# Performance work log

Measured on AMD Instinct MI355X. Metric: run time of the kernel, lower is better.

Reference implementation:

```python
import jax, jax.numpy as jnp
import numpy as np

N_NODES = 100000
N_EDGES = 1_600_000
D = 64


def setup_inputs() -> dict:
    key = jax.random.key(0)
    ks = jax.random.split(key, 10)
    features = jax.random.normal(ks[0], (N_NODES, D), dtype=jnp.float32)
    src = jax.random.randint(ks[1], (N_EDGES,), 0, N_NODES, dtype=jnp.int64)
    dst = jax.random.randint(ks[2], (N_EDGES,), 0, N_NODES, dtype=jnp.int64)
    s = 1.0 / np.sqrt(D)
    W0 = jax.random.uniform(ks[3], (D, D), jnp.float32, -s, s)
    b0 = jnp.zeros((D,), jnp.float32)
    W1 = jax.random.uniform(ks[4], (D, D), jnp.float32, -s, s)
    b1 = jnp.zeros((D,), jnp.float32)
    W2 = jax.random.uniform(ks[5], (D, D), jnp.float32, -s, s)
    b2 = jnp.zeros((D,), jnp.float32)
    return {"features": features, "src": src, "dst": dst,
            "W0": W0, "b0": b0, "W1": W1, "b1": b1, "W2": W2, "b2": b2}


def _graph_conv_left(h, src, dst, deg_inv, W, b, act):
    # norm='left': scale source features by 1/out_degree, then copy-sum aggregate
    h = h * deg_inv[:, None]          # [N, d]
    msgs = h[src]                     # [E, d] gather
    agg = jax.ops.segment_sum(msgs, dst, num_segments=N_NODES)  # [N, d]
    out = agg @ W + b
    return act(out) if act is not None else out


def reference(features, src, dst, W0, b0, W1, b1, W2, b2):
    # out-degree with clamp(min=1), as in DGL GraphConv
    deg = jax.ops.segment_sum(jnp.ones((N_EDGES,), jnp.float32), src,
                              num_segments=N_NODES)
    deg_inv = 1.0 / jnp.maximum(deg, 1.0)
    h = _graph_conv_left(features, src, dst, deg_inv, W0, b0, jax.nn.relu)
    h = _graph_conv_left(h, src, dst, deg_inv, W1, b1, jax.nn.relu)
    h = _graph_conv_left(h, src, dst, deg_inv, W2, b2, None)
    mN = jnp.mean(h, axis=0, keepdims=True)  # readout_nodes op='mean', single graph -> [1, d]
    return (h, mN)
```

## Files before the change

### kernel.cpp

```cpp
#include <hip/hip_runtime.h>
#include <hip/hip_fp16.h>

#define D 64
#define NBUK 391
#define NBIN (2 * NBUK)
#define CHUNK 8192
#define PBSTRIDE 256

__global__ __launch_bounds__(256) void phase1_kernel(const int* __restrict__ src,
                                                     const int* __restrict__ dst,
                                                     int* __restrict__ per_block, int E) {
    __shared__ int h[NBIN];
    int tid = (int)threadIdx.x;
    for (int j = tid; j < NBIN; j += 256) h[j] = 0;
    __syncthreads();
    int base = blockIdx.x * CHUNK;
    int cnt = min(CHUNK, E - base);
    for (int k = tid * 4; k < cnt; k += 1024) {
        if (k + 3 < cnt) {
            int4 d4 = *(const int4*)(dst + base + k);
            int4 s4 = *(const int4*)(src + base + k);
            atomicAdd(&h[d4.x >> 8], 1); atomicAdd(&h[d4.y >> 8], 1);
            atomicAdd(&h[d4.z >> 8], 1); atomicAdd(&h[d4.w >> 8], 1);
            atomicAdd(&h[NBUK + (s4.x >> 8)], 1); atomicAdd(&h[NBUK + (s4.y >> 8)], 1);
            atomicAdd(&h[NBUK + (s4.z >> 8)], 1); atomicAdd(&h[NBUK + (s4.w >> 8)], 1);
        } else {
            int kend = (k + 4 < cnt) ? k + 4 : cnt;
            for (int t = k; t < kend; ++t) {
                atomicAdd(&h[dst[base + t] >> 8], 1);
                atomicAdd(&h[NBUK + (src[base + t] >> 8)], 1);
            }
        }
    }
    __syncthreads();
    for (int j = tid; j < NBIN; j += 256) per_block[j * PBSTRIDE + blockIdx.x] = h[j];
}

__global__ __launch_bounds__(256) void scanA_kernel(int* __restrict__ per_block,
                                                    int* __restrict__ total) {
    int wv = (int)threadIdx.x >> 6;
    int lane = (int)threadIdx.x & 63;
    int j = blockIdx.x * 4 + wv;
    if (j >= NBIN) return;
    int* pb = per_block + (size_t)j * PBSTRIDE;
    int4 v = *(const int4*)(pb + lane * 4);
    int s1 = v.x + v.y, s2 = s1 + v.z, s3 = s2 + v.w;
    int x = s3;
#pragma unroll
    for (int d = 1; d < 64; d <<= 1) {
        int t = __shfl_up(x, d);
        if (lane >= d) x += t;
    }
    int excl = x - s3;
    int4 r = make_int4(excl, excl + v.x, excl + s1, excl + s2);
    *(int4*)(pb + lane * 4) = r;
    if (lane == 63) total[j] = x;
}

__global__ __launch_bounds__(512) void scanB_kernel(const int* __restrict__ total,
                                                    int* __restrict__ cb_dst,
                                                    int* __restrict__ cb_src) {
    __shared__ int s[512];
    int tid = (int)threadIdx.x;
    for (int half = 0; half < 2; ++half) {
        int v = (tid < NBUK) ? total[half * NBUK + tid] : 0;
        s[tid] = v;
        __syncthreads();
        for (int off = 1; off < 512; off <<= 1) {
            int t = (tid >= off) ? s[tid - off] : 0;
            __syncthreads();
            s[tid] += t;
            __syncthreads();
        }
        int* cb = half ? cb_src : cb_dst;
        if (tid < NBUK) cb[tid] = s[tid] - v;
        if (tid == NBUK - 1) cb[NBUK] = s[tid];
        __syncthreads();
    }
}

__global__ __launch_bounds__(256) void phase2_kernel(const int* __restrict__ src,
                                                     const int* __restrict__ dst,
                                                     const int* __restrict__ per_block,
                                                     const int* __restrict__ cb_dst,
                                                     const int* __restrict__ cb_src,
                                                     int* __restrict__ pairs,
                                                     unsigned char* __restrict__ skeys, int E) {
    __shared__ int lcur[NBIN];
    int tid = (int)threadIdx.x;
    for (int j = tid; j < NBIN; j += 256)
        lcur[j] = per_block[(size_t)j * PBSTRIDE + blockIdx.x] +
                  (j < NBUK ? cb_dst[j] : cb_src[j - NBUK]);
    __syncthreads();
    int base = blockIdx.x * CHUNK;
    int cnt = min(CHUNK, E - base);
    for (int k = tid * 4; k < cnt; k += 1024) {
        if (k + 3 < cnt) {
            int4 d4 = *(const int4*)(dst + base + k);
            int4 s4 = *(const int4*)(src + base + k);
            int p;
            p = atomicAdd(&lcur[d4.x >> 8], 1); pairs[p] = (s4.x << 8) | (d4.x & 255);
            p = atomicAdd(&lcur[d4.y >> 8], 1); pairs[p] = (s4.y << 8) | (d4.y & 255);
            p = atomicAdd(&lcur[d4.z >> 8], 1); pairs[p] = (s4.z << 8) | (d4.z & 255);
            p = atomicAdd(&lcur[d4.w >> 8], 1); pairs[p] = (s4.w << 8) | (d4.w & 255);
            p = atomicAdd(&lcur[NBUK + (s4.x >> 8)], 1); skeys[p] = (unsigned char)(s4.x & 255);
            p = atomicAdd(&lcur[NBUK + (s4.y >> 8)], 1); skeys[p] = (unsigned char)(s4.y & 255);
            p = atomicAdd(&lcur[NBUK + (s4.z >> 8)], 1); skeys[p] = (unsigned char)(s4.z & 255);
            p = atomicAdd(&lcur[NBUK + (s4.w >> 8)], 1); skeys[p] = (unsigned char)(s4.w & 255);
        } else {
            int kend = (k + 4 < cnt) ? k + 4 : cnt;
            for (int t = k; t < kend; ++t) {
                int dv = dst[base + t], sv = src[base + t];
                int p = atomicAdd(&lcur[dv >> 8], 1);
                pairs[p] = (sv << 8) | (dv & 255);
                p = atomicAdd(&lcur[NBUK + (sv >> 8)], 1);
                skeys[p] = (unsigned char)(sv & 255);
            }
        }
    }
}

__global__ __launch_bounds__(256) void finalize_csr_kernel(const int* __restrict__ pairs,
                                                           const unsigned char* __restrict__ skeys,
                                                           const int* __restrict__ cb_dst,
                                                           const int* __restrict__ cb_src,
                                                           int* __restrict__ row_ptr,
                                                           int* __restrict__ col,
                                                           float* __restrict__ dinv, int N) {
    __shared__ int fine[256];
    __shared__ int lcur[256];
    __shared__ int wtot[4], wexcl[4];
    int b = (int)blockIdx.x;
    int tid = (int)threadIdx.x, lane = tid & 63, wv = tid >> 6;
    int g = b * 256 + tid;

    fine[tid] = 0;
    __syncthreads();
    int sb0 = cb_src[b], sb1 = cb_src[b + 1];
    for (int i = sb0 + tid; i < sb1; i += 256) atomicAdd(&fine[skeys[i]], 1);
    __syncthreads();
    if (g < N) dinv[g] = 1.0f / fmaxf((float)fine[tid], 1.0f);
    __syncthreads();

    fine[tid] = 0;
    __syncthreads();
    int cb0 = cb_dst[b], cb1 = cb_dst[b + 1];
    for (int i = cb0 + tid; i < cb1; i += 256) atomicAdd(&fine[pairs[i] & 255], 1);
    __syncthreads();
    int v = fine[tid], x = v;
#pragma unroll
    for (int d = 1; d < 64; d <<= 1) {
        int t = __shfl_up(x, d);
        if (lane >= d) x += t;
    }
    if (lane == 63) wtot[wv] = x;
    __syncthreads();
    if (tid == 0) {
        int a = 0;
#pragma unroll
        for (int k = 0; k < 4; ++k) { wexcl[k] = a; a += wtot[k]; }
    }
    __syncthreads();
    int excl = x - v + wexcl[wv];
    if (g <= N) row_ptr[g] = cb0 + excl;
    lcur[tid] = cb0 + excl;
    __syncthreads();
    for (int i = cb0 + tid; i < cb1; i += 256) {
        int p = pairs[i];
        int pos = atomicAdd(&lcur[p & 255], 1);
        col[pos] = p >> 8;
    }
}

__global__ __launch_bounds__(256) void prescale_kernel(const float* __restrict__ feat,
                                                       const float* __restrict__ dinv,
                                                       __half* __restrict__ hs, int total8) {
    int i = blockIdx.x * 256 + threadIdx.x;
    if (i >= total8) return;
    int n = i >> 3;
    float sc = dinv[n];
    float4 v0 = ((const float4*)feat)[i * 2];
    float4 v1 = ((const float4*)feat)[i * 2 + 1];
    __half2 h[4];
    h[0] = __floats2half2_rn(v0.x * sc, v0.y * sc);
    h[1] = __floats2half2_rn(v0.z * sc, v0.w * sc);
    h[2] = __floats2half2_rn(v1.x * sc, v1.y * sc);
    h[3] = __floats2half2_rn(v1.z * sc, v1.w * sc);
    *(float4*)(hs + (size_t)i * 8) = *(float4*)h;
}

__device__ inline void accum8(float* a, float4 raw) {
    __half2* h = (__half2*)&raw;
#pragma unroll
    for (int k = 0; k < 4; ++k) {
        float2 f = __half22float2(h[k]);
        a[2 * k] += f.x;
        a[2 * k + 1] += f.y;
    }
}

__global__ __launch_bounds__(256) void fused_kernel(const __half* __restrict__ hs_in,
                                                    const int* __restrict__ row_ptr,
                                                    const int* __restrict__ col,
                                                    const float* __restrict__ W,
                                                    const float* __restrict__ bias,
                                                    const float* __restrict__ dinv,
                                                    float* __restrict__ outf,
                                                    __half* __restrict__ outh,
                                                    float* __restrict__ msum,
                                                    int N, int mode) {
    int tid = (int)threadIdx.x;
    int lane = tid & 63;
    int wv = tid >> 6;
    int sg = lane >> 3;
    int q = lane & 7;
    int g = wv * 8 + sg;

    float Wreg[64];
#pragma unroll
    for (int k = 0; k < 64; ++k) Wreg[k] = W[k * 64 + lane];
    float breg = bias[lane];

    __shared__ float aggT[32][68];

    int tile = blockIdx.x;
    int node_g = tile * 32 + g;
    float a[8];
#pragma unroll
    for (int k = 0; k < 8; ++k) a[k] = 0.0f;
    if (node_g < N) {
        int beg = row_ptr[node_g], end = row_ptr[node_g + 1];
        int j = beg;
        for (; j + 7 < end; j += 8) {
            int s0 = col[j], s1 = col[j + 1], s2 = col[j + 2], s3 = col[j + 3];
            int s4 = col[j + 4], s5 = col[j + 5], s6 = col[j + 6], s7 = col[j + 7];
            float4 r0 = *(const float4*)(hs_in + (size_t)s0 * D + q * 8);
            float4 r1 = *(const float4*)(hs_in + (size_t)s1 * D + q * 8);
            float4 r2 = *(const float4*)(hs_in + (size_t)s2 * D + q * 8);
            float4 r3 = *(const float4*)(hs_in + (size_t)s3 * D + q * 8);
            float4 r4 = *(const float4*)(hs_in + (size_t)s4 * D + q * 8);
            float4 r5 = *(const float4*)(hs_in + (size_t)s5 * D + q * 8);
            float4 r6 = *(const float4*)(hs_in + (size_t)s6 * D + q * 8);
            float4 r7 = *(const float4*)(hs_in + (size_t)s7 * D + q * 8);
            accum8(a, r0); accum8(a, r1); accum8(a, r2); accum8(a, r3);
            accum8(a, r4); accum8(a, r5); accum8(a, r6); accum8(a, r7);
        }
        for (; j < end; ++j) {
            int s0 = col[j];
            float4 r0 = *(const float4*)(hs_in + (size_t)s0 * D + q * 8);
            accum8(a, r0);
        }
    }
    *(float4*)(&aggT[g][q * 8]) = make_float4(a[0], a[1], a[2], a[3]);
    *(float4*)(&aggT[g][q * 8 + 4]) = make_float4(a[4], a[5], a[6], a[7]);

    float colacc = 0.0f;
#pragma unroll
    for (int rr = 0; rr < 8; ++rr) {
        int r = wv * 8 + rr;
        int node = tile * 32 + r;
        if (node < N) {
            float acc = breg;
            const float4* Ar = (const float4*)(&aggT[r][0]);
#pragma unroll
            for (int k4 = 0; k4 < 16; ++k4) {
                float4 av = Ar[k4];
                acc = fmaf(av.x, Wreg[k4 * 4 + 0], acc);
                acc = fmaf(av.y, Wreg[k4 * 4 + 1], acc);
                acc = fmaf(av.z, Wreg[k4 * 4 + 2], acc);
                acc = fmaf(av.w, Wreg[k4 * 4 + 3], acc);
            }
            if (mode == 0) {
                acc = fmaxf(acc, 0.0f) * dinv[node];
                outh[(size_t)node * D + lane] = __float2half(acc);
            } else {
                colacc += acc;
                outf[(size_t)node * D + lane] = acc;
            }
        }
    }

    if (mode == 1) {
        __shared__ float red[256];
        red[tid] = colacc;
        __syncthreads();
        if (wv == 0) {
            float s = red[lane] + red[64 + lane] + red[128 + lane] + red[192 + lane];
            atomicAdd(&msum[lane], s);
        }
    }
}

__global__ void finalize_kernel(const float* __restrict__ msum, float* __restrict__ outMean,
                                float invN) {
    outMean[threadIdx.x] = msum[threadIdx.x] * invN;
}

extern "C" void kernel_launch(void* const* d_in, const int* in_sizes, int n_in,
                              void* d_out, int out_size, void* d_ws, size_t ws_size,
                              hipStream_t stream) {
    const float* feat = (const float*)d_in[0];
    const int* src = (const int*)d_in[1];
    const int* dst = (const int*)d_in[2];
    const float* W0 = (const float*)d_in[3];
    const float* b0 = (const float*)d_in[4];
    const float* W1 = (const float*)d_in[5];
    const float* b1 = (const float*)d_in[6];
    const float* W2 = (const float*)d_in[7];
    const float* b2 = (const float*)d_in[8];

    const int N = in_sizes[0] / D;
    const int E = in_sizes[1];
    float* out = (float*)d_out;

    const int NBLK = (E + CHUNK - 1) / CHUNK;

    int* wsi = (int*)d_ws;
    const size_t NA = 100352;
    int*   row_ptr  = wsi;
    float* dinv     = (float*)(wsi + NA);
    float* msum     = (float*)(wsi + 2 * NA);
    int*   total    = wsi + 2 * NA + 256;
    int*   cb_dst   = wsi + 2 * NA + 1280;
    int*   cb_src   = wsi + 2 * NA + 1792;
    int*   per_blk  = wsi + 2 * NA + 2304;
    int*   pairs    = wsi + 2 * NA + 203008;
    unsigned char* skeys = (unsigned char*)(pairs + (size_t)E);
    int*   col      = pairs + (size_t)E + 400000;
    __half* hsA     = (__half*)(col + (size_t)E);
    __half* hsB     = hsA + (size_t)N * D;

    hipMemsetAsync(msum, 0, sizeof(float) * D, stream);
    hipMemsetAsync(per_blk, 0, sizeof(int) * (size_t)NBIN * PBSTRIDE, stream);

    phase1_kernel<<<NBLK, 256, 0, stream>>>(src, dst, per_blk, E);
    scanA_kernel<<<(NBIN + 3) / 4, 256, 0, stream>>>(per_blk, total);
    scanB_kernel<<<1, 512, 0, stream>>>(total, cb_dst, cb_src);
    phase2_kernel<<<NBLK, 256, 0, stream>>>(src, dst, per_blk, cb_dst, cb_src, pairs, skeys, E);
    finalize_csr_kernel<<<NBUK, 256, 0, stream>>>(pairs, skeys, cb_dst, cb_src, row_ptr, col, dinv, N);

    prescale_kernel<<<(N * 8 + 255) / 256, 256, 0, stream>>>(feat, dinv, hsA, N * 8);

    const int FG = (N + 31) / 32;
    fused_kernel<<<FG, 256, 0, stream>>>(hsA, row_ptr, col, W0, b0, dinv, nullptr, hsB, msum, N, 0);
    fused_kernel<<<FG, 256, 0, stream>>>(hsB, row_ptr, col, W1, b1, dinv, nullptr, hsA, msum, N, 0);
    fused_kernel<<<FG, 256, 0, stream>>>(hsA, row_ptr, col, W2, b2, dinv, out, nullptr, msum, N, 1);

    finalize_kernel<<<1, 64, 0, stream>>>(msum, out + (size_t)N * D, 1.0f / (float)N);
}
```

Before: 381.6 us.

## Fuse prescale into CSR finalize, pack weights as half2, use persistent fused blocks

Folds the feature prescale into the CSR finalize kernel, so degree inverses come from shared memory and one launch is removed. In the fused GCN kernel, weights are held as 32 half2 registers instead of 64 floats to cut register pressure and raise occupancy. The grid becomes a persistent 2048-block grid-stride loop over tiles, and the gather unroll drops from 8 to 4. Half-precision weights reduce accuracy and need extra converts, and the smaller unroll lowers memory-level parallelism per thread.

```diff
diff --git a/kernel.cpp b/kernel.cpp
--- a/kernel.cpp
+++ b/kernel.cpp
@@ -124,11 +124,14 @@
                                                            const unsigned char* __restrict__ skeys,
                                                            const int* __restrict__ cb_dst,
                                                            const int* __restrict__ cb_src,
+                                                           const float* __restrict__ feat,
                                                            int* __restrict__ row_ptr,
                                                            int* __restrict__ col,
-                                                           float* __restrict__ dinv, int N) {
+                                                           float* __restrict__ dinv,
+                                                           __half* __restrict__ hs, int N) {
     __shared__ int fine[256];
     __shared__ int lcur[256];
+    __shared__ float dsh[256];
     __shared__ int wtot[4], wexcl[4];
     int b = (int)blockIdx.x;
     int tid = (int)threadIdx.x, lane = tid & 63, wv = tid >> 6;
@@ -139,7 +142,30 @@
     int sb0 = cb_src[b], sb1 = cb_src[b + 1];
     for (int i = sb0 + tid; i < sb1; i += 256) atomicAdd(&fine[skeys[i]], 1);
     __syncthreads();
-    if (g < N) dinv[g] = 1.0f / fmaxf((float)fine[tid], 1.0f);
+    float dv_ = 1.0f / fmaxf((float)fine[tid], 1.0f);
+    dsh[tid] = dv_;
+    if (g < N) dinv[g] = dv_;
+    __syncthreads();
+
+    {
+        int q = tid & 7;
+        int rbase = tid >> 3;
+        for (int p = 0; p < 8; ++p) {
+            int r = p * 32 + rbase;
+            int node = b * 256 + r;
+            if (node < N) {
+                float sc = dsh[r];
+                const float4* f = (const float4*)(feat + (size_t)node * D + q * 8);
+                float4 v0 = f[0], v1 = f[1];
+                __half2 h[4];
+                h[0] = __floats2half2_rn(v0.x * sc, v0.y * sc);
+                h[1] = __floats2half2_rn(v0.z * sc, v0.w * sc);
+                h[2] = __floats2half2_rn(v1.x * sc, v1.y * sc);
+                h[3] = __floats2half2_rn(v1.z * sc, v1.w * sc);
+                *(float4*)(hs + (size_t)node * D + q * 8) = *(float4*)h;
+            }
+        }
+    }
     __syncthreads();
 
     fine[tid] = 0;
@@ -170,23 +196,6 @@
         int pos = atomicAdd(&lcur[p & 255], 1);
         col[pos] = p >> 8;
     }
-}
-
-__global__ __launch_bounds__(256) void prescale_kernel(const float* __restrict__ feat,
-                                                       const float* __restrict__ dinv,
-                                                       __half* __restrict__ hs, int total8) {
-    int i = blockIdx.x * 256 + threadIdx.x;
-    if (i >= total8) return;
-    int n = i >> 3;
-    float sc = dinv[n];
-    float4 v0 = ((const float4*)feat)[i * 2];
-    float4 v1 = ((const float4*)feat)[i * 2 + 1];
-    __half2 h[4];
-    h[0] = __floats2half2_rn(v0.x * sc, v0.y * sc);
-    h[1] = __floats2half2_rn(v0.z * sc, v0.w * sc);
-    h[2] = __floats2half2_rn(v1.x * sc, v1.y * sc);
-    h[3] = __floats2half2_rn(v1.z * sc, v1.w * sc);
-    *(float4*)(hs + (size_t)i * 8) = *(float4*)h;
 }
 
 __device__ inline void accum8(float* a, float4 raw) {
@@ -216,66 +225,65 @@
     int q = lane & 7;
     int g = wv * 8 + sg;
 
-    float Wreg[64];
-#pragma unroll
-    for (int k = 0; k < 64; ++k) Wreg[k] = W[k * 64 + lane];
+    __half2 Wreg[32];
+#pragma unroll
+    for (int k = 0; k < 32; ++k)
+        Wreg[k] = __floats2half2_rn(W[(2 * k) * 64 + lane], W[(2 * k + 1) * 64 + lane]);
     float breg = bias[lane];
 
     __shared__ float aggT[32][68];
-
-    int tile = blockIdx.x;
-    int node_g = tile * 32 + g;
-    float a[8];
-#pragma unroll
-    for (int k = 0; k < 8; ++k) a[k] = 0.0f;
-    if (node_g < N) {
-        int beg = row_ptr[node_g], end = row_ptr[node_g + 1];
-        int j = beg;
-        for (; j + 7 < end; j += 8) {
-            int s0 = col[j], s1 = col[j + 1], s2 = col[j + 2], s3 = col[j + 3];
-            int s4 = col[j + 4], s5 = col[j + 5], s6 = col[j + 6], s7 = col[j + 7];
-            float4 r0 = *(const float4*)(hs_in + (size_t)s0 * D + q * 8);
-            float4 r1 = *(const float4*)(hs_in + (size_t)s1 * D + q * 8);
-            float4 r2 = *(const float4*)(hs_in + (size_t)s2 * D + q * 8);
-            float4 r3 = *(const float4*)(hs_in + (size_t)s3 * D + q * 8);
-            float4 r4 = *(const float4*)(hs_in + (size_t)s4 * D + q * 8);
-            float4 r5 = *(const float4*)(hs_in + (size_t)s5 * D + q * 8);
-            float4 r6 = *(const float4*)(hs_in + (size_t)s6 * D + q * 8);
-            float4 r7 = *(const float4*)(hs_in + (size_t)s7 * D + q * 8);
-            accum8(a, r0); accum8(a, r1); accum8(a, r2); accum8(a, r3);
-            accum8(a, r4); accum8(a, r5); accum8(a, r6); accum8(a, r7);
-        }
-        for (; j < end; ++j) {
-            int s0 = col[j];
-            float4 r0 = *(const float4*)(hs_in + (size_t)s0 * D + q * 8);
-            accum8(a, r0);
-        }
-    }
-    *(float4*)(&aggT[g][q * 8]) = make_float4(a[0], a[1], a[2], a[3]);
-    *(float4*)(&aggT[g][q * 8 + 4]) = make_float4(a[4], a[5], a[6], a[7]);
-
     float colacc = 0.0f;
-#pragma unroll
-    for (int rr = 0; rr < 8; ++rr) {
-        int r = wv * 8 + rr;
-        int node = tile * 32 + r;
-        if (node < N) {
-            float acc = breg;
-            const float4* Ar = (const float4*)(&aggT[r][0]);
-#pragma unroll
-            for (int k4 = 0; k4 < 16; ++k4) {
-                float4 av = Ar[k4];
-                acc = fmaf(av.x, Wreg[k4 * 4 + 0], acc);
-                acc = fmaf(av.y, Wreg[k4 * 4 + 1], acc);
-                acc = fmaf(av.z, Wreg[k4 * 4 + 2], acc);
-                acc = fmaf(av.w, Wreg[k4 * 4 + 3], acc);
-            }
-            if (mode == 0) {
-                acc = fmaxf(acc, 0.0f) * dinv[node];
-                outh[(size_t)node * D + lane] = __float2half(acc);
-            } else {
-                colacc += acc;
-                outf[(size_t)node * D + lane] = acc;
+
+    int ntiles = (N + 31) >> 5;
+    for (int tile = blockIdx.x; tile < ntiles; tile += gridDim.x) {
+        int node_g = tile * 32 + g;
+        float a[8];
+#pragma unroll
+        for (int k = 0; k < 8; ++k) a[k] = 0.0f;
+        if (node_g < N) {
+            int beg = row_ptr[node_g], end = row_ptr[node_g + 1];
+            int j = beg;
+            for (; j + 3 < end; j += 4) {
+                int s0 = col[j], s1 = col[j + 1], s2 = col[j + 2], s3 = col[j + 3];
+                float4 r0 = *(const float4*)(hs_in + (size_t)s0 * D + q * 8);
+                float4 r1 = *(const float4*)(hs_in + (size_t)s1 * D + q * 8);
+                float4 r2 = *(const float4*)(hs_in + (size_t)s2 * D + q * 8);
+                float4 r3 = *(const float4*)(hs_in + (size_t)s3 * D + q * 8);
+                accum8(a, r0); accum8(a, r1); accum8(a, r2); accum8(a, r3);
+            }
+            for (; j < end; ++j) {
+                int s0 = col[j];
+                float4 r0 = *(const float4*)(hs_in + (size_t)s0 * D + q * 8);
+                accum8(a, r0);
+            }
+        }
+        *(float4*)(&aggT[g][q * 8]) = make_float4(a[0], a[1], a[2], a[3]);
+        *(float4*)(&aggT[g][q * 8 + 4]) = make_float4(a[4], a[5], a[6], a[7]);
+
+#pragma unroll
+        for (int rr = 0; rr < 8; ++rr) {
+            int r = wv * 8 + rr;
+            int node = tile * 32 + r;
+            if (node < N) {
+                float acc = breg;
+                const float4* Ar = (const float4*)(&aggT[r][0]);
+#pragma unroll
+                for (int k4 = 0; k4 < 16; ++k4) {
+                    float4 av = Ar[k4];
+                    __half2 w01 = Wreg[k4 * 2];
+                    __half2 w23 = Wreg[k4 * 2 + 1];
+                    acc = fmaf(av.x, __low2float(w01), acc);
+                    acc = fmaf(av.y, __high2float(w01), acc);
+                    acc = fmaf(av.z, __low2float(w23), acc);
+                    acc = fmaf(av.w, __high2float(w23), acc);
+                }
+                if (mode == 0) {
+                    acc = fmaxf(acc, 0.0f) * dinv[node];
+                    outh[(size_t)node * D + lane] = __float2half(acc);
+                } else {
+                    colacc += acc;
+                    outf[(size_t)node * D + lane] = acc;
+                }
             }
         }
     }
@@ -337,11 +345,10 @@
     scanA_kernel<<<(NBIN + 3) / 4, 256, 0, stream>>>(per_blk, total);
     scanB_kernel<<<1, 512, 0, stream>>>(total, cb_dst, cb_src);
     phase2_kernel<<<NBLK, 256, 0, stream>>>(src, dst, per_blk, cb_dst, cb_src, pairs, skeys, E);
-    finalize_csr_kernel<<<NBUK, 256, 0, stream>>>(pairs, skeys, cb_dst, cb_src, row_ptr, col, dinv, N);
-
-    prescale_kernel<<<(N * 8 + 255) / 256, 256, 0, stream>>>(feat, dinv, hsA, N * 8);
-
-    const int FG = (N + 31) / 32;
+    finalize_csr_kernel<<<NBUK, 256, 0, stream>>>(pairs, skeys, cb_dst, cb_src, feat,
+                                                  row_ptr, col, dinv, hsA, N);
+
+    const int FG = 2048;
     fused_kernel<<<FG, 256, 0, stream>>>(hsA, row_ptr, col, W0, b0, dinv, nullptr, hsB, msum, N, 0);
     fused_kernel<<<FG, 256, 0, stream>>>(hsB, row_ptr, col, W1, b1, dinv, nullptr, hsA, msum, N, 0);
     fused_kernel<<<FG, 256, 0, stream>>>(hsA, row_ptr, col, W2, b2, dinv, out, nullptr, msum, N, 1);
```

After: 341.9 us. -10.4%, faster.
